# Kernel optimization log

Hardware: AMD Instinct MI355X
Metric: run time of the kernel (lower is better)

## Reference

```python
import jax, jax.numpy as jnp
import numpy as np

B, L, D = 8, 4096, 256
H, C = 2, 128
DEG = 16  # incoming ring neighbors per node (excluding self loop)


def _build_edge_index():
    # Block-diagonal graph replicated per batch element, like _get_buffer.
    i = np.arange(L)
    offs = np.arange(1, DEG + 1)
    src_g = ((i[:, None] + offs[None, :]) % L).reshape(-1)   # [L*DEG]
    dst_g = np.repeat(i, DEG)                                 # [L*DEG]
    base = (np.arange(B) * L)[:, None]
    src = (src_g[None, :] + base).reshape(-1)
    dst = (dst_g[None, :] + base).reshape(-1)
    # PyG GATConv: remove_self_loops + add_self_loops -> exactly one self loop/node
    self_idx = np.arange(B * L)
    src = np.concatenate([src, self_idx])
    dst = np.concatenate([dst, self_idx])
    return jnp.asarray(np.stack([src, dst]), dtype=jnp.int32)  # [2, E]


def setup_inputs() -> dict:
    key = jax.random.key(0)
    k0, k1, k2, k3 = jax.random.split(key, 4)
    glorot = 1.0 / np.sqrt(D)
    return {
        "x": jax.random.normal(k0, (B, L, D), jnp.float32),
        "edge_index": _build_edge_index(),
        "W": jax.random.normal(k1, (D, H * C), jnp.float32) * glorot,
        "att_src": jax.random.normal(k2, (H, C), jnp.float32) * (1.0 / np.sqrt(C)),
        "att_dst": jax.random.normal(k3, (H, C), jnp.float32) * (1.0 / np.sqrt(C)),
        "bias": jnp.zeros((H * C,), jnp.float32),
    }


def reference(x, edge_index, W, att_src, att_dst, bias):
    b, l, d = x.shape
    n = b * l
    h_, c_ = att_src.shape
    xf = x.reshape(n, d)                                   # flatten batch of graphs
    res = xf
    h = (xf @ W).reshape(n, h_, c_)                        # [N,H,C] projected features
    a_src = jnp.einsum('nhc,hc->nh', h, att_src)           # per-node src logits
    a_dst = jnp.einsum('nhc,hc->nh', h, att_dst)
    s, t = edge_index[0], edge_index[1]
    alpha = jax.nn.leaky_relu(a_src[s] + a_dst[t], 0.2)    # [E,H]
    # softmax over incoming edges of each destination node
    amax = jax.ops.segment_max(alpha, t, num_segments=n)
    ex = jnp.exp(alpha - amax[t])
    denom = jax.ops.segment_sum(ex, t, num_segments=n)
    attn = ex / jnp.where(denom[t] > 0, denom[t], 1.0)     # [E,H]
    msg = h[s] * attn[:, :, None]                          # [E,H,C]
    out = jax.ops.segment_sum(msg, t, num_segments=n).reshape(n, h_ * c_) + bias
    out = jax.nn.relu(out) + res                           # relu + residual
    return out.reshape(b, l, h_ * c_)
```

## Files before the change

### kernel.cpp

```cpp
#include <hip/hip_runtime.h>

#define LL 4096
#define DD 256
#define TM 32
#define HALO 16
#define ROWS (TM + HALO)
#define NTH 256
#define APAD 40
#define HTS 56
#define WBS 40
#define ABUF_BYTES (ROWS * APAD * 2)

typedef float f32x4 __attribute__((ext_vector_type(4)));
typedef __bf16 bf16x8 __attribute__((ext_vector_type(8)));
typedef unsigned short us8 __attribute__((ext_vector_type(8)));
typedef unsigned short us4 __attribute__((ext_vector_type(4)));

__device__ __forceinline__ unsigned short f2bf(float f) {
    union { float f; unsigned u; } v; v.f = f;
    unsigned r = v.u + 0x7fffu + ((v.u >> 16) & 1u);
    return (unsigned short)(r >> 16);
}

#define KBAR() do {                                         \
    asm volatile("s_waitcnt lgkmcnt(0)" ::: "memory");      \
    __builtin_amdgcn_s_barrier();                           \
} while (0)

__global__ void prep_w(const float* __restrict__ W, unsigned short* __restrict__ Wt) {
    int t = blockIdx.x * blockDim.x + threadIdx.x;
    int l = t & 63;
    int kk = (t >> 6) & 7;
    int ct = t >> 9;
    int col = (ct << 4) + (l & 15);
    int kbase = kk * 32 + ((l >> 4) << 3);
    us8 v;
    for (int j = 0; j < 8; ++j) v[j] = f2bf(W[(kbase + j) * 256 + col]);
    *reinterpret_cast<us8*>(Wt + t * 8) = v;
}

__global__ __launch_bounds__(NTH, 4) void gat_fused(
    const float* __restrict__ x, const unsigned short* __restrict__ Wt,
    const float* __restrict__ att_src, const float* __restrict__ att_dst,
    const float* __restrict__ bias, float* __restrict__ out)
{
    __shared__ unsigned short h_t[256][HTS];
    __shared__ float alog[ROWS][2][2];
    __shared__ __align__(16) unsigned char smem_u[2 * ABUF_BYTES];
    unsigned short (*abuf0)[APAD] = reinterpret_cast<unsigned short(*)[APAD]>(smem_u);
    unsigned short (*abuf1)[APAD] = reinterpret_cast<unsigned short(*)[APAD]>(smem_u + ABUF_BYTES);
    unsigned short (*wband)[WBS]  = reinterpret_cast<unsigned short(*)[WBS]>(smem_u);

    const int tid  = threadIdx.x;
    const int lane = tid & 63;
    const int wv   = tid >> 6;
    const int lo   = lane & 15;
    const int hi   = lane >> 4;
    const int blk  = blockIdx.x;
    const int batch = blk >> 7;
    const int i0    = (blk & 127) * TM;
    const long xbase = (long)batch * (LL * DD);
    const int ct0 = wv * 4;
    const int hd  = wv >> 1;

    if (tid < 192) ((float*)alog)[tid] = 0.f;

    f32x4 acc[3][4];
    for (int a = 0; a < 3; ++a)
        for (int b = 0; b < 4; ++b)
            acc[a][b] = (f32x4){0.f, 0.f, 0.f, 0.f};

    const int s0r = tid >> 3, s0k = (tid & 7) << 2;
    const int s1r = (tid + 256) >> 3, s1k = (tid & 7) << 2;
    const float* xrow0 = x + xbase + (long)((i0 + s0r) & (LL - 1)) * DD + s0k;
    const float* xrow1 = x + xbase + (long)((i0 + s1r) & (LL - 1)) * DD + s1k;
    const unsigned short* wtb0 = Wt + (size_t)((ct0 + 0) * 8 * 64 + lane) * 8;
    const unsigned short* wtb1 = Wt + (size_t)((ct0 + 1) * 8 * 64 + lane) * 8;
    const unsigned short* wtb2 = Wt + (size_t)((ct0 + 2) * 8 * 64 + lane) * 8;
    const unsigned short* wtb3 = Wt + (size_t)((ct0 + 3) * 8 * 64 + lane) * 8;

    float4 cur0, cur1, nxt0, nxt1;
    us8 braw0, braw1, braw2, braw3;

    cur0 = *reinterpret_cast<const float4*>(xrow0);
    if (tid < 128) cur1 = *reinterpret_cast<const float4*>(xrow1);
    braw0 = *reinterpret_cast<const us8*>(wtb0);
    braw1 = *reinterpret_cast<const us8*>(wtb1);
    braw2 = *reinterpret_cast<const us8*>(wtb2);
    braw3 = *reinterpret_cast<const us8*>(wtb3);
    {
        us4 p;
        p[0] = f2bf(cur0.x); p[1] = f2bf(cur0.y); p[2] = f2bf(cur0.z); p[3] = f2bf(cur0.w);
        *reinterpret_cast<us4*>(&abuf0[s0r][s0k]) = p;
        if (tid < 128) {
            us4 q;
            q[0] = f2bf(cur1.x); q[1] = f2bf(cur1.y); q[2] = f2bf(cur1.z); q[3] = f2bf(cur1.w);
            *reinterpret_cast<us4*>(&abuf0[s1r][s1k]) = q;
        }
    }

#pragma unroll
    for (int kk = 0; kk < 8; ++kk) {
        unsigned short (*buf)[APAD]  = (kk & 1) ? abuf1 : abuf0;
        unsigned short (*nbuf)[APAD] = (kk & 1) ? abuf0 : abuf1;
        if (kk < 7) {
            nxt0 = *reinterpret_cast<const float4*>(xrow0 + (kk + 1) * 32);
            if (tid < 128) nxt1 = *reinterpret_cast<const float4*>(xrow1 + (kk + 1) * 32);
        }
        KBAR();

        bf16x8 bf0 = __builtin_bit_cast(bf16x8, braw0);
        bf16x8 bf1 = __builtin_bit_cast(bf16x8, braw1);
        bf16x8 bf2 = __builtin_bit_cast(bf16x8, braw2);
        bf16x8 bf3 = __builtin_bit_cast(bf16x8, braw3);
        for (int rt = 0; rt < 3; ++rt) {
            us8 araw = *reinterpret_cast<const us8*>(&buf[rt * 16 + lo][hi * 8]);
            bf16x8 afrag = __builtin_bit_cast(bf16x8, araw);
            acc[rt][0] = __builtin_amdgcn_mfma_f32_16x16x32_bf16(bf0, afrag, acc[rt][0], 0, 0, 0);
            acc[rt][1] = __builtin_amdgcn_mfma_f32_16x16x32_bf16(bf1, afrag, acc[rt][1], 0, 0, 0);
            acc[rt][2] = __builtin_amdgcn_mfma_f32_16x16x32_bf16(bf2, afrag, acc[rt][2], 0, 0, 0);
            acc[rt][3] = __builtin_amdgcn_mfma_f32_16x16x32_bf16(bf3, afrag, acc[rt][3], 0, 0, 0);
        }

        if (kk < 7) {
            braw0 = *reinterpret_cast<const us8*>(wtb0 + (size_t)(kk + 1) * 512);
            braw1 = *reinterpret_cast<const us8*>(wtb1 + (size_t)(kk + 1) * 512);
            braw2 = *reinterpret_cast<const us8*>(wtb2 + (size_t)(kk + 1) * 512);
            braw3 = *reinterpret_cast<const us8*>(wtb3 + (size_t)(kk + 1) * 512);
            us4 p;
            p[0] = f2bf(nxt0.x); p[1] = f2bf(nxt0.y); p[2] = f2bf(nxt0.z); p[3] = f2bf(nxt0.w);
            *reinterpret_cast<us4*>(&nbuf[s0r][s0k]) = p;
            if (tid < 128) {
                us4 q;
                q[0] = f2bf(nxt1.x); q[1] = f2bf(nxt1.y); q[2] = f2bf(nxt1.z); q[3] = f2bf(nxt1.w);
                *reinterpret_cast<us4*>(&nbuf[s1r][s1k]) = q;
            }
        }
    }

    {
        float4 as[4], ad[4];
#pragma unroll
        for (int c = 0; c < 4; ++c) {
            as[c] = *reinterpret_cast<const float4*>(att_src + (ct0 + c) * 16 + hi * 4);
            ad[c] = *reinterpret_cast<const float4*>(att_dst + (ct0 + c) * 16 + hi * 4);
        }
        float ps[3], pd[3];
        for (int rt = 0; rt < 3; ++rt) {
            ps[rt] = 0.f; pd[rt] = 0.f;
            int xrow = rt * 16 + lo;
#pragma unroll
            for (int c = 0; c < 4; ++c) {
                f32x4 a = acc[rt][c];
                ps[rt] += a[0] * as[c].x + a[1] * as[c].y + a[2] * as[c].z + a[3] * as[c].w;
                pd[rt] += a[0] * ad[c].x + a[1] * ad[c].y + a[2] * ad[c].z + a[3] * ad[c].w;
                for (int j = 0; j < 4; ++j)
                    h_t[(ct0 + c) * 16 + hi * 4 + j][xrow] = f2bf(a[j]);
            }
        }
        for (int rt = 0; rt < 3; ++rt) {
            ps[rt] += __shfl_xor(ps[rt], 16);
            ps[rt] += __shfl_xor(ps[rt], 32);
            pd[rt] += __shfl_xor(pd[rt], 16);
            pd[rt] += __shfl_xor(pd[rt], 32);
        }
        if (hi == 0) {
            for (int rt = 0; rt < 3; ++rt) {
                atomicAdd(&alog[rt * 16 + lo][hd][0], ps[rt]);
                atomicAdd(&alog[rt * 16 + lo][hd][1], pd[rt]);
            }
        }
    }

    float4 res[2][4];
    for (int ti = 0; ti < 2; ++ti)
        for (int c = 0; c < 4; ++c)
            res[ti][c] = *reinterpret_cast<const float4*>(
                x + xbase + (long)(i0 + ti * 16 + lo) * DD + (ct0 + c) * 16 + hi * 4);

    __syncthreads();

    if (tid < 64) {
        int r = tid >> 1, h2 = tid & 1;
        unsigned short* wrow = &wband[h2 * 32 + r][0];
        us8 z = {0, 0, 0, 0, 0, 0, 0, 0};
        for (int q = 0; q < 5; ++q) *reinterpret_cast<us8*>(wrow + q * 8) = z;
        float ad = alog[r][h2][1];
        float al[17];
        float mx = -1e30f;
        for (int k = 0; k < 17; ++k) {
            float s = (k < 16) ? alog[r + 1 + k][h2][0] : alog[r][h2][0];
            float v = s + ad;
            v = (v > 0.f) ? v : 0.2f * v;
            al[k] = v;
            mx = fmaxf(mx, v);
        }
        float sum = 0.f;
        for (int k = 0; k < 17; ++k) { al[k] = __expf(al[k] - mx); sum += al[k]; }
        float inv = 1.f / sum;
        int lo_r = r & 15;
        wrow[lo_r] = f2bf(al[16] * inv);
        for (int k = 0; k < 16; ++k) wrow[lo_r + 1 + k] = f2bf(al[k] * inv);
    }
    __syncthreads();

    {
        f32x4 acc2[2][4];
        for (int a = 0; a < 2; ++a)
            for (int b = 0; b < 4; ++b)
                acc2[a][b] = (f32x4){0.f, 0.f, 0.f, 0.f};

        for (int ti = 0; ti < 2; ++ti) {
            us8 raw = *reinterpret_cast<const us8*>(&wband[hd * 32 + ti * 16 + lo][hi * 8]);
            bf16x8 bfr = __builtin_bit_cast(bf16x8, raw);
#pragma unroll
            for (int c = 0; c < 4; ++c) {
                us8 araw = *reinterpret_cast<const us8*>(
                    &h_t[(ct0 + c) * 16 + lo][ti * 16 + hi * 8]);
                bf16x8 afr = __builtin_bit_cast(bf16x8, araw);
                acc2[ti][c] = __builtin_amdgcn_mfma_f32_16x16x32_bf16(afr, bfr, acc2[ti][c], 0, 0, 0);
            }
        }

        for (int ti = 0; ti < 2; ++ti)
#pragma unroll
            for (int c = 0; c < 4; ++c) {
                const float4 b4 = *reinterpret_cast<const float4*>(bias + (ct0 + c) * 16 + hi * 4);
                f32x4 s = acc2[ti][c];
                long g = xbase + (long)(i0 + ti * 16 + lo) * DD + (ct0 + c) * 16 + hi * 4;
                float4 o;
                o.x = fmaxf(s[0] + b4.x, 0.f) + res[ti][c].x;
                o.y = fmaxf(s[1] + b4.y, 0.f) + res[ti][c].y;
                o.z = fmaxf(s[2] + b4.z, 0.f) + res[ti][c].z;
                o.w = fmaxf(s[3] + b4.w, 0.f) + res[ti][c].w;
                *reinterpret_cast<float4*>(out + g) = o;
            }
    }
}

extern "C" void kernel_launch(void* const* d_in, const int* in_sizes, int n_in,
                              void* d_out, int out_size, void* d_ws, size_t ws_size,
                              hipStream_t stream) {
    const float* x       = (const float*)d_in[0];
    const float* W       = (const float*)d_in[2];
    const float* att_src = (const float*)d_in[3];
    const float* att_dst = (const float*)d_in[4];
    const float* bias    = (const float*)d_in[5];
    float* out           = (float*)d_out;
    unsigned short* Wt   = (unsigned short*)d_ws;

    hipLaunchKernelGGL(prep_w, dim3(128), dim3(64), 0, stream, W, Wt);
    hipLaunchKernelGGL(gat_fused, dim3(1024), dim3(NTH), 0, stream,
                       x, Wt, att_src, att_dst, bias, out);
}
```

Before: 30.07 us.

## Split fused GAT kernel into projection GEMM and aggregation kernels via global buffer

Replaces the single fused kernel, which recomputed a 16-row halo of projected features per tile, with two kernels. The first computes h for each 32-node tile and stores it transposed in bf16 to a workspace, along with per-node attention logits. The second reads the halo features and logits from global memory to do the softmax and aggregation. This removes the redundant halo GEMM work, at the cost of an extra launch and an extra global round trip for h and the logits.

Result: slower. 46.02 us (+53.0%).

```diff
diff --git a/kernel.cpp b/kernel.cpp
--- a/kernel.cpp
+++ b/kernel.cpp
@@ -3,13 +3,11 @@
 #define LL 4096
 #define DD 256
 #define TM 32
-#define HALO 16
-#define ROWS (TM + HALO)
 #define NTH 256
 #define APAD 40
-#define HTS 56
+#define HTS 40
 #define WBS 40
-#define ABUF_BYTES (ROWS * APAD * 2)
+#define NNODE 32768
 
 typedef float f32x4 __attribute__((ext_vector_type(4)));
 typedef __bf16 bf16x8 __attribute__((ext_vector_type(8)));
@@ -39,17 +37,15 @@
     *reinterpret_cast<us8*>(Wt + t * 8) = v;
 }
 
-__global__ __launch_bounds__(NTH, 4) void gat_fused(
+__global__ __launch_bounds__(NTH, 4) void gat_gemm(
     const float* __restrict__ x, const unsigned short* __restrict__ Wt,
     const float* __restrict__ att_src, const float* __restrict__ att_dst,
-    const float* __restrict__ bias, float* __restrict__ out)
+    unsigned short* __restrict__ hTg, float* __restrict__ alog_g)
 {
+    __shared__ unsigned short abuf0[TM][APAD];
+    __shared__ unsigned short abuf1[TM][APAD];
     __shared__ unsigned short h_t[256][HTS];
-    __shared__ float alog[ROWS][2][2];
-    __shared__ __align__(16) unsigned char smem_u[2 * ABUF_BYTES];
-    unsigned short (*abuf0)[APAD] = reinterpret_cast<unsigned short(*)[APAD]>(smem_u);
-    unsigned short (*abuf1)[APAD] = reinterpret_cast<unsigned short(*)[APAD]>(smem_u + ABUF_BYTES);
-    unsigned short (*wband)[WBS]  = reinterpret_cast<unsigned short(*)[WBS]>(smem_u);
+    __shared__ float alog[TM][2][2];
 
     const int tid  = threadIdx.x;
     const int lane = tid & 63;
@@ -59,31 +55,29 @@
     const int blk  = blockIdx.x;
     const int batch = blk >> 7;
     const int i0    = (blk & 127) * TM;
+    const int n0    = blk * TM;
     const long xbase = (long)batch * (LL * DD);
     const int ct0 = wv * 4;
     const int hd  = wv >> 1;
 
-    if (tid < 192) ((float*)alog)[tid] = 0.f;
-
-    f32x4 acc[3][4];
-    for (int a = 0; a < 3; ++a)
+    if (tid < 128) ((float*)alog)[tid] = 0.f;
+
+    f32x4 acc[2][4];
+    for (int a = 0; a < 2; ++a)
         for (int b = 0; b < 4; ++b)
             acc[a][b] = (f32x4){0.f, 0.f, 0.f, 0.f};
 
     const int s0r = tid >> 3, s0k = (tid & 7) << 2;
-    const int s1r = (tid + 256) >> 3, s1k = (tid & 7) << 2;
-    const float* xrow0 = x + xbase + (long)((i0 + s0r) & (LL - 1)) * DD + s0k;
-    const float* xrow1 = x + xbase + (long)((i0 + s1r) & (LL - 1)) * DD + s1k;
+    const float* xrow0 = x + xbase + (long)(i0 + s0r) * DD + s0k;
     const unsigned short* wtb0 = Wt + (size_t)((ct0 + 0) * 8 * 64 + lane) * 8;
     const unsigned short* wtb1 = Wt + (size_t)((ct0 + 1) * 8 * 64 + lane) * 8;
     const unsigned short* wtb2 = Wt + (size_t)((ct0 + 2) * 8 * 64 + lane) * 8;
     const unsigned short* wtb3 = Wt + (size_t)((ct0 + 3) * 8 * 64 + lane) * 8;
 
-    float4 cur0, cur1, nxt0, nxt1;
+    float4 cur0, nxt0;
     us8 braw0, braw1, braw2, braw3;
 
     cur0 = *reinterpret_cast<const float4*>(xrow0);
-    if (tid < 128) cur1 = *reinterpret_cast<const float4*>(xrow1);
     braw0 = *reinterpret_cast<const us8*>(wtb0);
     braw1 = *reinterpret_cast<const us8*>(wtb1);
     braw2 = *reinterpret_cast<const us8*>(wtb2);
@@ -92,28 +86,21 @@
         us4 p;
         p[0] = f2bf(cur0.x); p[1] = f2bf(cur0.y); p[2] = f2bf(cur0.z); p[3] = f2bf(cur0.w);
         *reinterpret_cast<us4*>(&abuf0[s0r][s0k]) = p;
-        if (tid < 128) {
-            us4 q;
-            q[0] = f2bf(cur1.x); q[1] = f2bf(cur1.y); q[2] = f2bf(cur1.z); q[3] = f2bf(cur1.w);
-            *reinterpret_cast<us4*>(&abuf0[s1r][s1k]) = q;
-        }
     }
 
 #pragma unroll
     for (int kk = 0; kk < 8; ++kk) {
         unsigned short (*buf)[APAD]  = (kk & 1) ? abuf1 : abuf0;
         unsigned short (*nbuf)[APAD] = (kk & 1) ? abuf0 : abuf1;
-        if (kk < 7) {
+        if (kk < 7)
             nxt0 = *reinterpret_cast<const float4*>(xrow0 + (kk + 1) * 32);
-            if (tid < 128) nxt1 = *reinterpret_cast<const float4*>(xrow1 + (kk + 1) * 32);
-        }
         KBAR();
 
         bf16x8 bf0 = __builtin_bit_cast(bf16x8, braw0);
         bf16x8 bf1 = __builtin_bit_cast(bf16x8, braw1);
         bf16x8 bf2 = __builtin_bit_cast(bf16x8, braw2);
         bf16x8 bf3 = __builtin_bit_cast(bf16x8, braw3);
-        for (int rt = 0; rt < 3; ++rt) {
+        for (int rt = 0; rt < 2; ++rt) {
             us8 araw = *reinterpret_cast<const us8*>(&buf[rt * 16 + lo][hi * 8]);
             bf16x8 afrag = __builtin_bit_cast(bf16x8, araw);
             acc[rt][0] = __builtin_amdgcn_mfma_f32_16x16x32_bf16(bf0, afrag, acc[rt][0], 0, 0, 0);
@@ -130,11 +117,6 @@
             us4 p;
             p[0] = f2bf(nxt0.x); p[1] = f2bf(nxt0.y); p[2] = f2bf(nxt0.z); p[3] = f2bf(nxt0.w);
             *reinterpret_cast<us4*>(&nbuf[s0r][s0k]) = p;
-            if (tid < 128) {
-                us4 q;
-                q[0] = f2bf(nxt1.x); q[1] = f2bf(nxt1.y); q[2] = f2bf(nxt1.z); q[3] = f2bf(nxt1.w);
-                *reinterpret_cast<us4*>(&nbuf[s1r][s1k]) = q;
-            }
         }
     }
 
@@ -145,8 +127,8 @@
             as[c] = *reinterpret_cast<const float4*>(att_src + (ct0 + c) * 16 + hi * 4);
             ad[c] = *reinterpret_cast<const float4*>(att_dst + (ct0 + c) * 16 + hi * 4);
         }
-        float ps[3], pd[3];
-        for (int rt = 0; rt < 3; ++rt) {
+        float ps[2], pd[2];
+        for (int rt = 0; rt < 2; ++rt) {
             ps[rt] = 0.f; pd[rt] = 0.f;
             int xrow = rt * 16 + lo;
 #pragma unroll
@@ -158,26 +140,64 @@
                     h_t[(ct0 + c) * 16 + hi * 4 + j][xrow] = f2bf(a[j]);
             }
         }
-        for (int rt = 0; rt < 3; ++rt) {
+        for (int rt = 0; rt < 2; ++rt) {
             ps[rt] += __shfl_xor(ps[rt], 16);
             ps[rt] += __shfl_xor(ps[rt], 32);
             pd[rt] += __shfl_xor(pd[rt], 16);
             pd[rt] += __shfl_xor(pd[rt], 32);
         }
         if (hi == 0) {
-            for (int rt = 0; rt < 3; ++rt) {
+            for (int rt = 0; rt < 2; ++rt) {
                 atomicAdd(&alog[rt * 16 + lo][hd][0], ps[rt]);
                 atomicAdd(&alog[rt * 16 + lo][hd][1], pd[rt]);
             }
         }
     }
+    __syncthreads();
+
+#pragma unroll
+    for (int p = 0; p < 8; ++p) {
+        int chan = p * 32 + (tid >> 3);
+        int seg  = tid & 7;
+        us4 v = *reinterpret_cast<const us4*>(&h_t[chan][seg * 4]);
+        *reinterpret_cast<us4*>(hTg + (size_t)chan * NNODE + n0 + seg * 4) = v;
+    }
+    if (tid < 128)
+        alog_g[(size_t)n0 * 4 + tid] = ((float*)alog)[tid];
+}
+
+__global__ __launch_bounds__(NTH, 4) void gat_agg(
+    const float* __restrict__ x, const unsigned short* __restrict__ hTg,
+    const float* __restrict__ alog_g, const float* __restrict__ bias,
+    float* __restrict__ out)
+{
+    __shared__ unsigned short wband[64][WBS];
+    __shared__ float alogl[48][2][2];
+
+    const int tid  = threadIdx.x;
+    const int lane = tid & 63;
+    const int wv   = tid >> 6;
+    const int lo   = lane & 15;
+    const int hi   = lane >> 4;
+    const int blk  = blockIdx.x;
+    const int batch = blk >> 7;
+    const int i0l   = (blk & 127) * TM;
+    const long xbase = (long)batch * (LL * DD);
+    const int ct0 = wv * 4;
+    const int hd  = wv >> 1;
 
     float4 res[2][4];
     for (int ti = 0; ti < 2; ++ti)
+#pragma unroll
         for (int c = 0; c < 4; ++c)
             res[ti][c] = *reinterpret_cast<const float4*>(
-                x + xbase + (long)(i0 + ti * 16 + lo) * DD + (ct0 + c) * 16 + hi * 4);
-
+                x + xbase + (long)(i0l + ti * 16 + lo) * DD + (ct0 + c) * 16 + hi * 4);
+
+    if (tid < 192) {
+        int r = tid >> 2, q = tid & 3;
+        long node = (long)batch * LL + ((i0l + r) & (LL - 1));
+        ((float*)alogl)[tid] = alog_g[node * 4 + q];
+    }
     __syncthreads();
 
     if (tid < 64) {
@@ -185,11 +205,11 @@
         unsigned short* wrow = &wband[h2 * 32 + r][0];
         us8 z = {0, 0, 0, 0, 0, 0, 0, 0};
         for (int q = 0; q < 5; ++q) *reinterpret_cast<us8*>(wrow + q * 8) = z;
-        float ad = alog[r][h2][1];
+        float ad = alogl[r][h2][1];
         float al[17];
         float mx = -1e30f;
         for (int k = 0; k < 17; ++k) {
-            float s = (k < 16) ? alog[r + 1 + k][h2][0] : alog[r][h2][0];
+            float s = (k < 16) ? alogl[r + 1 + k][h2][0] : alogl[r][h2][0];
             float v = s + ad;
             v = (v > 0.f) ? v : 0.2f * v;
             al[k] = v;
@@ -213,10 +233,11 @@
         for (int ti = 0; ti < 2; ++ti) {
             us8 raw = *reinterpret_cast<const us8*>(&wband[hd * 32 + ti * 16 + lo][hi * 8]);
             bf16x8 bfr = __builtin_bit_cast(bf16x8, raw);
+            long nbase = (long)batch * LL + ((i0l + ti * 16 + hi * 8) & (LL - 1));
 #pragma unroll
             for (int c = 0; c < 4; ++c) {
                 us8 araw = *reinterpret_cast<const us8*>(
-                    &h_t[(ct0 + c) * 16 + lo][ti * 16 + hi * 8]);
+                    hTg + (size_t)((ct0 + c) * 16 + lo) * NNODE + nbase);
                 bf16x8 afr = __builtin_bit_cast(bf16x8, araw);
                 acc2[ti][c] = __builtin_amdgcn_mfma_f32_16x16x32_bf16(afr, bfr, acc2[ti][c], 0, 0, 0);
             }
@@ -227,7 +248,7 @@
             for (int c = 0; c < 4; ++c) {
                 const float4 b4 = *reinterpret_cast<const float4*>(bias + (ct0 + c) * 16 + hi * 4);
                 f32x4 s = acc2[ti][c];
-                long g = xbase + (long)(i0 + ti * 16 + lo) * DD + (ct0 + c) * 16 + hi * 4;
+                long g = xbase + (long)(i0l + ti * 16 + lo) * DD + (ct0 + c) * 16 + hi * 4;
                 float4 o;
                 o.x = fmaxf(s[0] + b4.x, 0.f) + res[ti][c].x;
                 o.y = fmaxf(s[1] + b4.y, 0.f) + res[ti][c].y;
@@ -247,9 +268,14 @@
     const float* att_dst = (const float*)d_in[4];
     const float* bias    = (const float*)d_in[5];
     float* out           = (float*)d_out;
+
     unsigned short* Wt   = (unsigned short*)d_ws;
+    unsigned short* hTg  = (unsigned short*)((char*)d_ws + (256 << 10));
+    float* alog_g        = (float*)((char*)d_ws + (256 << 10) + (16 << 20));
 
     hipLaunchKernelGGL(prep_w, dim3(128), dim3(64), 0, stream, W, Wt);
-    hipLaunchKernelGGL(gat_fused, dim3(1024), dim3(NTH), 0, stream,
-                       x, Wt, att_src, att_dst, bias, out);
-}
+    hipLaunchKernelGGL(gat_gemm, dim3(1024), dim3(NTH), 0, stream,
+                       x, Wt, att_src, att_dst, hTg, alog_g);
+    hipLaunchKernelGGL(gat_agg, dim3(1024), dim3(NTH), 0, stream,
+                       x, hTg, alog_g, bias, out);
+}
```

## Stage whole x tile in LDS upfront and drop per-k barriers

Applied to the files above, without the earlier changes.

The kernel now loads the full 48-row by 256-column x tile into registers in one pass, converts it with packed v_cvt_pk_bf16_f32 instructions, and writes it to LDS behind a single barrier. This replaces the double-buffered, per-k-step staging that needed a barrier on every iteration; the GEMM loop then only prefetches W fragments. To fit LDS, the projected-feature transpose buffer now aliases the x tile, so its writes move after an extra barrier, and the attention band buffer gets its own allocation. The intent is fewer barriers and more memory-level parallelism on the x loads, in exchange for higher register pressure and a larger LDS footprint per block.

Result: slower. 38.08 us (+26.6%).

```diff
diff --git a/kernel.cpp b/kernel.cpp
--- a/kernel.cpp
+++ b/kernel.cpp
@@ -3,23 +3,28 @@
 #define LL 4096
 #define DD 256
 #define TM 32
-#define HALO 16
-#define ROWS (TM + HALO)
+#define ROWS 48
 #define NTH 256
-#define APAD 40
+#define XTS 264
 #define HTS 56
 #define WBS 40
-#define ABUF_BYTES (ROWS * APAD * 2)
 
 typedef float f32x4 __attribute__((ext_vector_type(4)));
 typedef __bf16 bf16x8 __attribute__((ext_vector_type(8)));
 typedef unsigned short us8 __attribute__((ext_vector_type(8)));
 typedef unsigned short us4 __attribute__((ext_vector_type(4)));
+typedef unsigned int u32x2 __attribute__((ext_vector_type(2)));
 
 __device__ __forceinline__ unsigned short f2bf(float f) {
     union { float f; unsigned u; } v; v.f = f;
     unsigned r = v.u + 0x7fffu + ((v.u >> 16) & 1u);
     return (unsigned short)(r >> 16);
+}
+
+__device__ __forceinline__ unsigned cvtpk_bf16(float a, float b) {
+    unsigned r;
+    asm("v_cvt_pk_bf16_f32 %0, %1, %2" : "=v"(r) : "v"(a), "v"(b));
+    return r;
 }
 
 #define KBAR() do {                                         \
@@ -44,12 +49,11 @@
     const float* __restrict__ att_src, const float* __restrict__ att_dst,
     const float* __restrict__ bias, float* __restrict__ out)
 {
-    __shared__ unsigned short h_t[256][HTS];
+    __shared__ __align__(16) unsigned short smem_u[256 * HTS];
+    unsigned short (*xbuf)[XTS] = reinterpret_cast<unsigned short(*)[XTS]>(smem_u);
+    unsigned short (*h_t)[HTS]  = reinterpret_cast<unsigned short(*)[HTS]>(smem_u);
+    __shared__ unsigned short wband[64][WBS];
     __shared__ float alog[ROWS][2][2];
-    __shared__ __align__(16) unsigned char smem_u[2 * ABUF_BYTES];
-    unsigned short (*abuf0)[APAD] = reinterpret_cast<unsigned short(*)[APAD]>(smem_u);
-    unsigned short (*abuf1)[APAD] = reinterpret_cast<unsigned short(*)[APAD]>(smem_u + ABUF_BYTES);
-    unsigned short (*wband)[WBS]  = reinterpret_cast<unsigned short(*)[WBS]>(smem_u);
 
     const int tid  = threadIdx.x;
     const int lane = tid & 63;
@@ -65,77 +69,61 @@
 
     if (tid < 192) ((float*)alog)[tid] = 0.f;
 
+    float4 xv[12];
+#pragma unroll
+    for (int s = 0; s < 12; ++s) {
+        int id = tid + s * NTH;
+        int row = id >> 6, c4 = (id & 63) << 2;
+        xv[s] = *reinterpret_cast<const float4*>(
+            x + xbase + (long)((i0 + row) & (LL - 1)) * DD + c4);
+    }
+    const unsigned short* wtb0 = Wt + (size_t)((ct0 + 0) * 8 * 64 + lane) * 8;
+    const unsigned short* wtb1 = Wt + (size_t)((ct0 + 1) * 8 * 64 + lane) * 8;
+    const unsigned short* wtb2 = Wt + (size_t)((ct0 + 2) * 8 * 64 + lane) * 8;
+    const unsigned short* wtb3 = Wt + (size_t)((ct0 + 3) * 8 * 64 + lane) * 8;
+    us8 br0 = *reinterpret_cast<const us8*>(wtb0);
+    us8 br1 = *reinterpret_cast<const us8*>(wtb1);
+    us8 br2 = *reinterpret_cast<const us8*>(wtb2);
+    us8 br3 = *reinterpret_cast<const us8*>(wtb3);
+
+#pragma unroll
+    for (int s = 0; s < 12; ++s) {
+        int id = tid + s * NTH;
+        int row = id >> 6, c4 = (id & 63) << 2;
+        u32x2 p;
+        p[0] = cvtpk_bf16(xv[s].x, xv[s].y);
+        p[1] = cvtpk_bf16(xv[s].z, xv[s].w);
+        *reinterpret_cast<u32x2*>(&xbuf[row][c4]) = p;
+    }
+    KBAR();
+
     f32x4 acc[3][4];
     for (int a = 0; a < 3; ++a)
         for (int b = 0; b < 4; ++b)
             acc[a][b] = (f32x4){0.f, 0.f, 0.f, 0.f};
 
-    const int s0r = tid >> 3, s0k = (tid & 7) << 2;
-    const int s1r = (tid + 256) >> 3, s1k = (tid & 7) << 2;
-    const float* xrow0 = x + xbase + (long)((i0 + s0r) & (LL - 1)) * DD + s0k;
-    const float* xrow1 = x + xbase + (long)((i0 + s1r) & (LL - 1)) * DD + s1k;
-    const unsigned short* wtb0 = Wt + (size_t)((ct0 + 0) * 8 * 64 + lane) * 8;
-    const unsigned short* wtb1 = Wt + (size_t)((ct0 + 1) * 8 * 64 + lane) * 8;
-    const unsigned short* wtb2 = Wt + (size_t)((ct0 + 2) * 8 * 64 + lane) * 8;
-    const unsigned short* wtb3 = Wt + (size_t)((ct0 + 3) * 8 * 64 + lane) * 8;
-
-    float4 cur0, cur1, nxt0, nxt1;
-    us8 braw0, braw1, braw2, braw3;
-
-    cur0 = *reinterpret_cast<const float4*>(xrow0);
-    if (tid < 128) cur1 = *reinterpret_cast<const float4*>(xrow1);
-    braw0 = *reinterpret_cast<const us8*>(wtb0);
-    braw1 = *reinterpret_cast<const us8*>(wtb1);
-    braw2 = *reinterpret_cast<const us8*>(wtb2);
-    braw3 = *reinterpret_cast<const us8*>(wtb3);
-    {
-        us4 p;
-        p[0] = f2bf(cur0.x); p[1] = f2bf(cur0.y); p[2] = f2bf(cur0.z); p[3] = f2bf(cur0.w);
-        *reinterpret_cast<us4*>(&abuf0[s0r][s0k]) = p;
-        if (tid < 128) {
-            us4 q;
-            q[0] = f2bf(cur1.x); q[1] = f2bf(cur1.y); q[2] = f2bf(cur1.z); q[3] = f2bf(cur1.w);
-            *reinterpret_cast<us4*>(&abuf0[s1r][s1k]) = q;
-        }
-    }
-
+    us8 nbr0, nbr1, nbr2, nbr3;
 #pragma unroll
     for (int kk = 0; kk < 8; ++kk) {
-        unsigned short (*buf)[APAD]  = (kk & 1) ? abuf1 : abuf0;
-        unsigned short (*nbuf)[APAD] = (kk & 1) ? abuf0 : abuf1;
         if (kk < 7) {
-            nxt0 = *reinterpret_cast<const float4*>(xrow0 + (kk + 1) * 32);
-            if (tid < 128) nxt1 = *reinterpret_cast<const float4*>(xrow1 + (kk + 1) * 32);
-        }
-        KBAR();
-
-        bf16x8 bf0 = __builtin_bit_cast(bf16x8, braw0);
-        bf16x8 bf1 = __builtin_bit_cast(bf16x8, braw1);
-        bf16x8 bf2 = __builtin_bit_cast(bf16x8, braw2);
-        bf16x8 bf3 = __builtin_bit_cast(bf16x8, braw3);
+            nbr0 = *reinterpret_cast<const us8*>(wtb0 + (size_t)(kk + 1) * 512);
+            nbr1 = *reinterpret_cast<const us8*>(wtb1 + (size_t)(kk + 1) * 512);
+            nbr2 = *reinterpret_cast<const us8*>(wtb2 + (size_t)(kk + 1) * 512);
+            nbr3 = *reinterpret_cast<const us8*>(wtb3 + (size_t)(kk + 1) * 512);
+        }
+        bf16x8 bf0 = __builtin_bit_cast(bf16x8, br0);
+        bf16x8 bf1 = __builtin_bit_cast(bf16x8, br1);
+        bf16x8 bf2 = __builtin_bit_cast(bf16x8, br2);
+        bf16x8 bf3 = __builtin_bit_cast(bf16x8, br3);
         for (int rt = 0; rt < 3; ++rt) {
-            us8 araw = *reinterpret_cast<const us8*>(&buf[rt * 16 + lo][hi * 8]);
+            us8 araw = *reinterpret_cast<const us8*>(&xbuf[rt * 16 + lo][kk * 32 + hi * 8]);
             bf16x8 afrag = __builtin_bit_cast(bf16x8, araw);
             acc[rt][0] = __builtin_amdgcn_mfma_f32_16x16x32_bf16(bf0, afrag, acc[rt][0], 0, 0, 0);
             acc[rt][1] = __builtin_amdgcn_mfma_f32_16x16x32_bf16(bf1, afrag, acc[rt][1], 0, 0, 0);
             acc[rt][2] = __builtin_amdgcn_mfma_f32_16x16x32_bf16(bf2, afrag, acc[rt][2], 0, 0, 0);
             acc[rt][3] = __builtin_amdgcn_mfma_f32_16x16x32_bf16(bf3, afrag, acc[rt][3], 0, 0, 0);
         }
-
-        if (kk < 7) {
-            braw0 = *reinterpret_cast<const us8*>(wtb0 + (size_t)(kk + 1) * 512);
-            braw1 = *reinterpret_cast<const us8*>(wtb1 + (size_t)(kk + 1) * 512);
-            braw2 = *reinterpret_cast<const us8*>(wtb2 + (size_t)(kk + 1) * 512);
-            braw3 = *reinterpret_cast<const us8*>(wtb3 + (size_t)(kk + 1) * 512);
-            us4 p;
-            p[0] = f2bf(nxt0.x); p[1] = f2bf(nxt0.y); p[2] = f2bf(nxt0.z); p[3] = f2bf(nxt0.w);
-            *reinterpret_cast<us4*>(&nbuf[s0r][s0k]) = p;
-            if (tid < 128) {
-                us4 q;
-                q[0] = f2bf(nxt1.x); q[1] = f2bf(nxt1.y); q[2] = f2bf(nxt1.z); q[3] = f2bf(nxt1.w);
-                *reinterpret_cast<us4*>(&nbuf[s1r][s1k]) = q;
-            }
-        }
+        if (kk < 7) { br0 = nbr0; br1 = nbr1; br2 = nbr2; br3 = nbr3; }
     }
 
     {
@@ -148,14 +136,11 @@
         float ps[3], pd[3];
         for (int rt = 0; rt < 3; ++rt) {
             ps[rt] = 0.f; pd[rt] = 0.f;
-            int xrow = rt * 16 + lo;
 #pragma unroll
             for (int c = 0; c < 4; ++c) {
                 f32x4 a = acc[rt][c];
                 ps[rt] += a[0] * as[c].x + a[1] * as[c].y + a[2] * as[c].z + a[3] * as[c].w;
                 pd[rt] += a[0] * ad[c].x + a[1] * ad[c].y + a[2] * ad[c].z + a[3] * ad[c].w;
-                for (int j = 0; j < 4; ++j)
-                    h_t[(ct0 + c) * 16 + hi * 4 + j][xrow] = f2bf(a[j]);
             }
         }
         for (int rt = 0; rt < 3; ++rt) {
@@ -172,13 +157,22 @@
         }
     }
 
+    KBAR();
+
+    for (int rt = 0; rt < 3; ++rt) {
+        int xrow = rt * 16 + lo;
+#pragma unroll
+        for (int c = 0; c < 4; ++c)
+            for (int j = 0; j < 4; ++j)
+                h_t[(ct0 + c) * 16 + hi * 4 + j][xrow] = f2bf(acc[rt][c][j]);
+    }
+
     float4 res[2][4];
     for (int ti = 0; ti < 2; ++ti)
+#pragma unroll
         for (int c = 0; c < 4; ++c)
             res[ti][c] = *reinterpret_cast<const float4*>(
                 x + xbase + (long)(i0 + ti * 16 + lo) * DD + (ct0 + c) * 16 + hi * 4);
-
-    __syncthreads();
 
     if (tid < 64) {
         int r = tid >> 1, h2 = tid & 1;
@@ -202,7 +196,8 @@
         wrow[lo_r] = f2bf(al[16] * inv);
         for (int k = 0; k < 16; ++k) wrow[lo_r + 1 + k] = f2bf(al[k] * inv);
     }
-    __syncthreads();
+
+    KBAR();
 
     {
         f32x4 acc2[2][4];
```
